# Kernel optimization log

Hardware: AMD Instinct MI355X
Metric: run time of the kernel (lower is better)

The kernel has to match this reference:

```python
import jax, jax.numpy as jnp
import numpy as np
import math

TOP_K = 2
CAPACITY_FACTOR = 1.25


def setup_inputs() -> dict:
    key = jax.random.key(0)
    ks = jax.random.split(key, 5)
    T, H, F, E = 16384, 1024, 4096, 8
    s = lambda d: 1.0 / np.sqrt(d)
    return {
        "tokens": jax.random.normal(ks[0], (T, H), jnp.float32),
        "w_router": jax.random.normal(ks[1], (H, E), jnp.float32) * s(H),
        "w_gate": jax.random.normal(ks[2], (E, H, F), jnp.float32) * s(H),
        "w_up": jax.random.normal(ks[3], (E, H, F), jnp.float32) * s(H),
        "w_down": jax.random.normal(ks[4], (E, F, H), jnp.float32) * s(F),
    }


def _moe_forward(tokens, w_router, w_gate, w_up, w_down):
    T, H = tokens.shape
    E = w_gate.shape[0]
    C = int(math.ceil(CAPACITY_FACTOR * T / E))  # per-expert capacity, static

    # --- Router: softmax over experts, top-k, renormalized weights ---
    logits = tokens @ w_router                       # (T, E)
    probs = jax.nn.softmax(logits, axis=-1)
    topv, topi = jax.lax.top_k(probs, TOP_K)         # (T, K)
    weights = topv / jnp.sum(topv, axis=-1, keepdims=True)

    # --- Dispatch ranks replicating torch loop order: k-slot major, token index minor ---
    onehot = jax.nn.one_hot(topi, E, dtype=jnp.int32)            # (T, K, E)
    counts = onehot.sum(axis=0)                                  # (K, E) tokens per (slot, expert)
    slot_off = jnp.concatenate(
        [jnp.zeros((1, E), jnp.int32), jnp.cumsum(counts, axis=0)[:-1]], axis=0
    )                                                            # (K, E) exclusive offset over k
    rank = jnp.cumsum(onehot, axis=0) - 1 + slot_off[None]       # (T, K, E)
    rank_tk = jnp.take_along_axis(rank, topi[..., None], axis=-1).squeeze(-1)  # (T, K)

    keep = rank_tk < C                                           # tokens beyond capacity are dropped
    slot = jnp.where(keep, rank_tk, C)                           # dropped -> trash slot C

    e_flat = topi.reshape(-1)                                    # (T*K,)
    s_flat = slot.reshape(-1)
    tok_rep = jnp.broadcast_to(tokens[:, None, :], (T, TOP_K, H)).reshape(-1, H)

    # Gather tokens into per-expert capacity buffers (extra trash row at slot C)
    buf = jnp.zeros((E, C + 1, H), tokens.dtype).at[e_flat, s_flat].set(tok_rep)
    x = buf[:, :C]                                               # (E, C, H)

    # --- SwiGLU expert FFN, batched over experts (grouped GEMM) ---
    h = jax.nn.silu(jnp.einsum('ech,ehf->ecf', x, w_gate)) * jnp.einsum('ech,ehf->ecf', x, w_up)
    y = jnp.einsum('ecf,efh->ech', h, w_down)                    # (E, C, H)

    # --- Weighted scatter back to token positions ---
    out_flat = y[e_flat, jnp.minimum(s_flat, C - 1)]             # (T*K, H)
    w_eff = (weights * keep.astype(weights.dtype)).reshape(-1, 1)
    return (out_flat * w_eff).reshape(T, TOP_K, H).sum(axis=1)   # (T, H)


def reference(tokens, w_router, w_gate, w_up, w_down):
    return _moe_forward(tokens, w_router, w_gate, w_up, w_down)
```

## Files before the change

### kernel.cpp

```cpp
#include <hip/hip_runtime.h>
#include <hip/hip_bf16.h>
#include <stdint.h>

#define T_TOK 16384
#define HDIM  1024
#define FDIM  4096
#define NE    8
#define CAP   2560

typedef __attribute__((ext_vector_type(8))) __bf16 bf16x8;
typedef __attribute__((ext_vector_type(4))) float  f32x4;

#define MFMA_BF16 __builtin_amdgcn_mfma_f32_16x16x32_bf16
#define VMCNT3()  asm volatile("s_waitcnt vmcnt(3)" ::: "memory")
#define VMCNT4()  asm volatile("s_waitcnt vmcnt(4)" ::: "memory")
#define LGKM0()   asm volatile("s_waitcnt lgkmcnt(0)" ::: "memory")
#define BAR()     __builtin_amdgcn_s_barrier()
#define SCHED0()  __builtin_amdgcn_sched_barrier(0)

__device__ __forceinline__ unsigned short f2bf(float f) {
  union { float f; unsigned u; } c; c.f = f;
  unsigned u = c.u;
  return (unsigned short)((u + 0x7FFFu + ((u >> 16) & 1u)) >> 16);
}

__device__ __forceinline__ float bf2f(unsigned short u) {
  union { unsigned u; float f; } c; c.u = ((unsigned)u) << 16;
  return c.f;
}

__device__ __forceinline__ void gload_lds16(const void* g, void* lds) {
  __builtin_amdgcn_global_load_lds((const __attribute__((address_space(1))) void*)g,
                                   (__attribute__((address_space(3))) void*)lds,
                                   16, 0, 0);
}

__global__ __launch_bounds__(256)
void transpose_cvt(const float* __restrict__ in, unsigned short* __restrict__ out,
                   int R, int Cc) {
  __shared__ unsigned short tile[64][68];
  int e  = blockIdx.z;
  int rb = blockIdx.y << 6, cb = blockIdx.x << 6;
  const float* inp = in + (size_t)e * R * Cc;
  unsigned short* op = out + (size_t)e * R * Cc;
  int lc  = threadIdx.x & 63;
  int lr0 = threadIdx.x >> 6;
#pragma unroll
  for (int rr = 0; rr < 64; rr += 4) {
    int r = rr + lr0;
    float v = inp[(size_t)(rb + r) * Cc + cb + lc];
    tile[lc][r] = f2bf(v);
  }
  __syncthreads();
  int c0 = threadIdx.x >> 3;
  int h0 = (threadIdx.x & 7) << 3;
#pragma unroll
  for (int cc = 0; cc < 64; cc += 32) {
    int c = cc + c0;
    uint2 v0 = *(const uint2*)&tile[c][h0];
    uint2 v1 = *(const uint2*)&tile[c][h0 + 4];
    uint4 v; v.x = v0.x; v.y = v0.y; v.z = v1.x; v.w = v1.y;
    *(uint4*)(op + (size_t)(cb + c) * R + rb + h0) = v;
  }
}

__global__ __launch_bounds__(256)
void transpose_cvt_gu(const float* __restrict__ in, unsigned short* __restrict__ out, int up) {
  __shared__ unsigned short tile[64][68];
  int e  = blockIdx.z;
  int rb = blockIdx.y << 6, cb = blockIdx.x << 6;
  const float* inp = in + (size_t)e * HDIM * FDIM;
  unsigned short* op = out + (size_t)e * 2 * FDIM * HDIM;
  int lc  = threadIdx.x & 63;
  int lr0 = threadIdx.x >> 6;
#pragma unroll
  for (int rr = 0; rr < 64; rr += 4) {
    int r = rr + lr0;
    float v = inp[(size_t)(rb + r) * FDIM + cb + lc];
    tile[lc][r] = f2bf(v);
  }
  __syncthreads();
  int c0 = threadIdx.x >> 3;
  int h0 = (threadIdx.x & 7) << 3;
#pragma unroll
  for (int cc = 0; cc < 64; cc += 32) {
    int c = cc + c0;
    int C = cb + c;
    int orow = ((C >> 5) << 6) + (C & 31) + (up << 5);
    uint2 v0 = *(const uint2*)&tile[c][h0];
    uint2 v1 = *(const uint2*)&tile[c][h0 + 4];
    uint4 v; v.x = v0.x; v.y = v0.y; v.z = v1.x; v.w = v1.y;
    *(uint4*)(op + (size_t)orow * HDIM + rb + h0) = v;
  }
}

__global__ __launch_bounds__(256)
void router_kernel(const float* __restrict__ tokens, const float* __restrict__ wr,
                   int* __restrict__ topsel, float* __restrict__ wts) {
  int lane = threadIdx.x & 63;
  int t = (blockIdx.x << 2) + (threadIdx.x >> 6);
  const float* tok = tokens + (size_t)t * HDIM;
  float acc[8];
#pragma unroll
  for (int i = 0; i < 8; ++i) acc[i] = 0.f;
#pragma unroll
  for (int j = 0; j < 4; ++j) {
    int h0 = j * 256 + lane * 4;
    float4 tv = *(const float4*)(tok + h0);
    const float* w = wr + (size_t)h0 * 8;
#pragma unroll
    for (int q = 0; q < 4; ++q) {
      float xv = ((const float*)&tv)[q];
      float4 wa = *(const float4*)(w + q * 8);
      float4 wb = *(const float4*)(w + q * 8 + 4);
      acc[0] += xv * wa.x; acc[1] += xv * wa.y; acc[2] += xv * wa.z; acc[3] += xv * wa.w;
      acc[4] += xv * wb.x; acc[5] += xv * wb.y; acc[6] += xv * wb.z; acc[7] += xv * wb.w;
    }
  }
#pragma unroll
  for (int off = 1; off < 64; off <<= 1) {
#pragma unroll
    for (int i = 0; i < 8; ++i) acc[i] += __shfl_xor(acc[i], off, 64);
  }
  if (lane == 0) {
    int e0 = 0; float v0 = acc[0];
#pragma unroll
    for (int i = 1; i < 8; ++i) if (acc[i] > v0) { v0 = acc[i]; e0 = i; }
    int e1 = -1; float v1 = -3.4e38f;
#pragma unroll
    for (int i = 0; i < 8; ++i) if (i != e0 && acc[i] > v1) { v1 = acc[i]; e1 = i; }
    float w0 = 1.f / (1.f + __expf(v1 - v0));
    topsel[t * 2] = e0; topsel[t * 2 + 1] = e1;
    wts[t * 2] = w0;    wts[t * 2 + 1] = 1.f - w0;
  }
}

__global__ __launch_bounds__(256)
void dispatch_kernel(const int* __restrict__ topsel, int* __restrict__ slot,
                     int* __restrict__ src_tok) {
  int e = blockIdx.x;
  int w = threadIdx.x >> 6, lane = threadIdx.x & 63;
  __shared__ int gcnt[2][256];
  __shared__ int tot[2];
#pragma unroll
  for (int k = 0; k < 2; ++k)
    for (int g = w; g < 256; g += 4) {
      int ch = topsel[(g * 64 + lane) * 2 + k];
      unsigned long long m = __ballot(ch == e);
      if (lane == 0) gcnt[k][g] = __popcll(m);
    }
  __syncthreads();
  if (w < 2) {
    int k = w;
    int c0 = gcnt[k][lane * 4], c1 = gcnt[k][lane * 4 + 1];
    int c2 = gcnt[k][lane * 4 + 2], c3 = gcnt[k][lane * 4 + 3];
    int s = c0 + c1 + c2 + c3;
    int inc = s;
#pragma unroll
    for (int off = 1; off < 64; off <<= 1) {
      int v = __shfl_up(inc, off, 64);
      if (lane >= off) inc += v;
    }
    int base = inc - s;
    gcnt[k][lane * 4] = base;
    gcnt[k][lane * 4 + 1] = base + c0;
    gcnt[k][lane * 4 + 2] = base + c0 + c1;
    gcnt[k][lane * 4 + 3] = base + c0 + c1 + c2;
    if (lane == 63) tot[k] = inc;
  }
  __syncthreads();
#pragma unroll
  for (int k = 0; k < 2; ++k) {
    int kbase = (k == 1) ? tot[0] : 0;
    for (int g = w; g < 256; g += 4) {
      int t = g * 64 + lane;
      int ch = topsel[t * 2 + k];
      unsigned long long m = __ballot(ch == e);
      if (ch == e) {
        unsigned long long lmask = lane ? (~0ull >> (64 - lane)) : 0ull;
        int r = kbase + gcnt[k][g] + __popcll(m & lmask);
        if (r < CAP) { slot[t * 2 + k] = r; src_tok[e * CAP + r] = t; }
        else         { slot[t * 2 + k] = -1; }
      }
    }
  }
}

__global__ __launch_bounds__(128)
void gather_x(const float* __restrict__ tokens, const int* __restrict__ src_tok,
              unsigned short* __restrict__ x) {
  int s = blockIdx.x;
  int t = src_tok[s];
  unsigned short* xr = x + (size_t)s * HDIM + threadIdx.x * 8;
  uint4 v = {0u, 0u, 0u, 0u};
  if (t >= 0) {
    const float* tr = tokens + (size_t)t * HDIM + threadIdx.x * 8;
    float4 a = *(const float4*)tr;
    float4 b = *(const float4*)(tr + 4);
    v.x = (unsigned)f2bf(a.x) | ((unsigned)f2bf(a.y) << 16);
    v.y = (unsigned)f2bf(a.z) | ((unsigned)f2bf(a.w) << 16);
    v.z = (unsigned)f2bf(b.x) | ((unsigned)f2bf(b.y) << 16);
    v.w = (unsigned)f2bf(b.z) | ((unsigned)f2bf(b.w) << 16);
  }
  *(uint4*)xr = v;
}

template<int BN>
__device__ __forceinline__ void mainloop8(const unsigned short* __restrict__ Ag,
                                          const unsigned short* __restrict__ Bg,
                                          int lda, int ldb, int nkt,
                                          unsigned short* lds, f32x4 (&acc)[4][BN / 32]) {
  constexpr int NF   = BN / 64;
  constexpr int AELB = 256 * 64 * 2;
  constexpr int BELB = BN * 64 * 2;
  constexpr int BHB  = (BN / 2) * 128;
  int tid = threadIdx.x, lane = tid & 63, wid = tid >> 6;
  int qr = wid >> 1, qc = wid & 1;
  int fr = lane & 15, fg = lane >> 4;

  char* ldsc = (char*)lds;
  int swz0 = ((fg       ^ (fr & 7)) << 4);
  int swz1 = (((4 | fg) ^ (fr & 7)) << 4);
  const char* a_b0 = ldsc + (qr * 32 + fr) * 128 + swz0;
  const char* a_b1 = ldsc + (qr * 32 + fr) * 128 + swz1;
  const char* b_b0 = ldsc + 2 * AELB + (qc * (NF * 16) + fr) * 128 + swz0;
  const char* b_b1 = ldsc + 2 * AELB + (qc * (NF * 16) + fr) * 128 + swz1;

  int srow = tid >> 3;
  int sl8  = ((tid & 7) ^ (srow & 7)) * 8;

  auto stA = [&](int mh, int kt, int pb) {
    char* dst = ldsc + pb + mh * 16384;
    gload_lds16(Ag + (size_t)(mh * 128 + srow) * lda + kt + sl8, dst + tid * 16);
    gload_lds16(Ag + (size_t)(mh * 128 + 64 + srow) * lda + kt + sl8, dst + tid * 16 + 8192);
  };
  auto stB = [&](int nh, int kt, int qb) {
    char* dst = ldsc + 2 * AELB + qb + nh * BHB;
    gload_lds16(Bg + (size_t)(nh * (BN / 2) + srow) * ldb + kt + sl8, dst + tid * 16);
    if constexpr (BN == 256)
      gload_lds16(Bg + (size_t)(nh * (BN / 2) + 64 + srow) * ldb + kt + sl8,
                  dst + tid * 16 + 8192);
  };

  bf16x8 aA[2][2], aB[2][2], bA[NF][2], bB[NF][2];
  auto rdA = [&](bf16x8 (&dst)[2][2], int mh, int pb) {
#pragma unroll
    for (int mf = 0; mf < 2; ++mf) {
      dst[mf][0] = *(const bf16x8*)(a_b0 + pb + mh * 16384 + mf * 2048);
      dst[mf][1] = *(const bf16x8*)(a_b1 + pb + mh * 16384 + mf * 2048);
    }
  };
  auto rdB = [&](bf16x8 (&dst)[NF][2], int nh, int qb) {
#pragma unroll
    for (int nf = 0; nf < NF; ++nf) {
      dst[nf][0] = *(const bf16x8*)(b_b0 + qb + nh * BHB + nf * 2048);
      dst[nf][1] = *(const bf16x8*)(b_b1 + qb + nh * BHB + nf * 2048);
    }
  };
  auto mmq = [&](bf16x8 (&A)[2][2], bf16x8 (&B)[NF][2], int mh, int nh) {
    __builtin_amdgcn_s_setprio(1);
#pragma unroll
    for (int kk = 0; kk < 2; ++kk)
#pragma unroll
      for (int mf = 0; mf < 2; ++mf)
#pragma unroll
        for (int nf = 0; nf < NF; ++nf)
          acc[mh * 2 + mf][nh * NF + nf] =
              MFMA_BF16(A[mf][kk], B[nf][kk], acc[mh * 2 + mf][nh * NF + nf], 0, 0, 0);
    __builtin_amdgcn_s_setprio(0);
  };

  int ktp = (nkt > 1 ? 64 : 0);
  stA(0, 0, 0); stB(0, 0, 0); stA(1, 0, 0); stB(1, 0, 0);
  stA(0, ktp, AELB); stB(1, ktp, BELB);
  if constexpr (BN == 256) VMCNT4(); else VMCNT3();
  BAR();

  for (int t = 0; t < nkt; ++t) {
    int p0 = (t & 1) ? AELB : 0, p1 = AELB - p0;
    int q0 = (t & 1) ? BELB : 0, q1 = BELB - q0;
    int kt1 = ((t + 1 < nkt) ? t + 1 : nkt - 1) * 64;
    int kt2 = ((t + 2 < nkt) ? t + 2 : nkt - 1) * 64;

    rdA(aA, 0, p0); rdB(bA, 0, q0); rdA(aB, 1, p0);
    stB(0, kt1, q1);
    SCHED0();
    LGKM0();
    mmq(aA, bA, 0, 0);
    BAR();

    rdB(bB, 1, q0);
    stA(1, kt1, p1);
    SCHED0();
    mmq(aB, bA, 1, 0);
    LGKM0();
    BAR();

    stA(0, kt2, p0);
    mmq(aB, bB, 1, 1);
    BAR();

    stB(1, kt2, q0);
    mmq(aA, bB, 0, 1);
    if constexpr (BN == 256) VMCNT4(); else VMCNT3();
    BAR();
  }
}

__global__ __launch_bounds__(512, 1)
void gemm1_kernel(const unsigned short* __restrict__ x, const unsigned short* __restrict__ wgu,
                  unsigned short* __restrict__ h) {
  __shared__ unsigned short lds[2 * 256 * 64 + 2 * 256 * 64];
  int flat = blockIdx.x;
  int e = flat & 7, idx = flat >> 3;
  int c = idx >> 4, i = idx & 15;
  int cbx = c / 5, cby = c % 5;
  int bx = cbx * 8 + (i & 7), by = cby * 2 + (i >> 3);
  const unsigned short* Ag = x   + ((size_t)e * CAP + (size_t)by * 256) * HDIM;
  const unsigned short* Bg = wgu + ((size_t)e * 2 * FDIM + (size_t)bx * 256) * HDIM;
  f32x4 acc[4][8];
#pragma unroll
  for (int m = 0; m < 4; ++m)
#pragma unroll
    for (int n = 0; n < 8; ++n) acc[m][n] = (f32x4){0.f, 0.f, 0.f, 0.f};
  mainloop8<256>(Ag, Bg, HDIM, HDIM, HDIM / 64, lds, acc);

  int lane = threadIdx.x & 63, wid = threadIdx.x >> 6;
  int qr = wid >> 1, qc = wid & 1, fr = lane & 15, fg = lane >> 4;
  size_t rbase = (size_t)e * CAP + by * 256;
#pragma unroll
  for (int mi = 0; mi < 4; ++mi) {
    int row0 = (mi >> 1) * 128 + qr * 32 + (mi & 1) * 16 + fg * 4;
#pragma unroll
    for (int nh = 0; nh < 2; ++nh)
#pragma unroll
      for (int nf = 0; nf < 2; ++nf) {
        int fcol = bx * 128 + (nh * 2 + qc) * 32 + nf * 16 + fr;
#pragma unroll
        for (int v = 0; v < 4; ++v) {
          float g = acc[mi][nh * 4 + nf][v];
          float u = acc[mi][nh * 4 + nf + 2][v];
          float s = g / (1.f + __expf(-g));
          h[(rbase + row0 + v) * FDIM + fcol] = f2bf(s * u);
        }
      }
  }
}

__global__ __launch_bounds__(512, 1)
void gemm2_kernel(const unsigned short* __restrict__ h, const unsigned short* __restrict__ wdT,
                  unsigned short* __restrict__ y0, unsigned short* __restrict__ y1) {
  __shared__ unsigned short lds[2 * 256 * 64 + 2 * 256 * 64];
  int flat = blockIdx.x;
  int e = flat & 7, idx = flat >> 3;
  int ks = idx & 1, r2 = idx >> 1;
  int bx = r2 & 3, by = r2 >> 2;
  int k0 = ks * 2048;
  const unsigned short* Ag = h   + ((size_t)e * CAP  + (size_t)by * 256) * FDIM + k0;
  const unsigned short* Bg = wdT + ((size_t)e * HDIM + (size_t)bx * 256) * FDIM + k0;
  f32x4 acc[4][8];
#pragma unroll
  for (int m = 0; m < 4; ++m)
#pragma unroll
    for (int n = 0; n < 8; ++n) acc[m][n] = (f32x4){0.f, 0.f, 0.f, 0.f};
  mainloop8<256>(Ag, Bg, FDIM, FDIM, 2048 / 64, lds, acc);

  unsigned short* yk = ks ? y1 : y0;
  int lane = threadIdx.x & 63, wid = threadIdx.x >> 6;
  int qr = wid >> 1, qc = wid & 1, fr = lane & 15, fg = lane >> 4;
  size_t rbase = (size_t)e * CAP + by * 256;
#pragma unroll
  for (int mi = 0; mi < 4; ++mi) {
    int row0 = (mi >> 1) * 128 + qr * 32 + (mi & 1) * 16 + fg * 4;
#pragma unroll
    for (int nh = 0; nh < 2; ++nh)
#pragma unroll
      for (int nf = 0; nf < 4; ++nf) {
        int col = bx * 256 + nh * 128 + qc * 64 + nf * 16 + fr;
#pragma unroll
        for (int v = 0; v < 4; ++v)
          yk[(rbase + row0 + v) * HDIM + col] = f2bf(acc[mi][nh * 4 + nf][v]);
      }
  }
}

__global__ __launch_bounds__(256)
void combine_kernel(const unsigned short* __restrict__ y0, const unsigned short* __restrict__ y1,
                    const int* __restrict__ topsel, const int* __restrict__ slot,
                    const float* __restrict__ wts, float* __restrict__ out) {
  int t = blockIdx.x;
  int i = threadIdx.x * 4;
  float4 s = {0.f, 0.f, 0.f, 0.f};
#pragma unroll
  for (int k = 0; k < 2; ++k) {
    int sl = slot[t * 2 + k];
    if (sl >= 0) {
      int e = topsel[t * 2 + k];
      float w = wts[t * 2 + k];
      size_t base = ((size_t)e * CAP + sl) * HDIM + i;
      uint2 a = *(const uint2*)(y0 + base);
      uint2 b = *(const uint2*)(y1 + base);
      s.x += w * (bf2f((unsigned short)(a.x & 0xFFFF)) + bf2f((unsigned short)(b.x & 0xFFFF)));
      s.y += w * (bf2f((unsigned short)(a.x >> 16))    + bf2f((unsigned short)(b.x >> 16)));
      s.z += w * (bf2f((unsigned short)(a.y & 0xFFFF)) + bf2f((unsigned short)(b.y & 0xFFFF)));
      s.w += w * (bf2f((unsigned short)(a.y >> 16))    + bf2f((unsigned short)(b.y >> 16)));
    }
  }
  *(float4*)(out + (size_t)t * HDIM + i) = s;
}

extern "C" void kernel_launch(void* const* d_in, const int* in_sizes, int n_in,
                              void* d_out, int out_size, void* d_ws, size_t ws_size,
                              hipStream_t stream) {
  const float* tokens   = (const float*)d_in[0];
  const float* w_router = (const float*)d_in[1];
  const float* w_gate   = (const float*)d_in[2];
  const float* w_up     = (const float*)d_in[3];
  const float* w_down   = (const float*)d_in[4];
  float* out = (float*)d_out;
  char* ws = (char*)d_ws;

  const size_t WGU = (size_t)NE * 2 * FDIM * HDIM * 2;
  const size_t WD  = (size_t)NE * HDIM * FDIM * 2;
  const size_t XB  = (size_t)NE * CAP * HDIM * 2;
  const size_t HB  = (size_t)NE * CAP * FDIM * 2;
  const size_t YB  = (size_t)NE * CAP * HDIM * 2;
  unsigned short* wguT = (unsigned short*)(ws);
  unsigned short* wdT  = (unsigned short*)(ws + WGU);
  unsigned short* xbuf = (unsigned short*)(ws + WGU + WD);
  unsigned short* hbuf = (unsigned short*)(ws + WGU + WD + XB);
  unsigned short* ybuf0 = (unsigned short*)(ws);
  unsigned short* ybuf1 = (unsigned short*)(ws + YB);
  char* tail = ws + WGU + WD + XB + HB;
  int*   topsel  = (int*)tail;
  float* wtsv    = (float*)(tail + (size_t)T_TOK * 2 * 4);
  int*   slotv   = (int*)(tail + (size_t)T_TOK * 2 * 8);
  int*   src_tok = (int*)(tail + (size_t)T_TOK * 2 * 12);

  hipMemsetAsync(src_tok, 0xFF, (size_t)NE * CAP * 4, stream);

  transpose_cvt_gu<<<dim3(FDIM / 64, HDIM / 64, NE), 256, 0, stream>>>(w_gate, wguT, 0);
  transpose_cvt_gu<<<dim3(FDIM / 64, HDIM / 64, NE), 256, 0, stream>>>(w_up,   wguT, 1);
  transpose_cvt<<<dim3(HDIM / 64, FDIM / 64, NE), 256, 0, stream>>>(w_down, wdT, FDIM, HDIM);

  router_kernel<<<T_TOK / 4, 256, 0, stream>>>(tokens, w_router, topsel, wtsv);
  dispatch_kernel<<<NE, 256, 0, stream>>>(topsel, slotv, src_tok);
  gather_x<<<NE * CAP, 128, 0, stream>>>(tokens, src_tok, xbuf);

  gemm1_kernel<<<2560, 512, 0, stream>>>(xbuf, wguT, hbuf);
  gemm2_kernel<<<640, 512, 0, stream>>>(hbuf, wdT, ybuf0, ybuf1);

  combine_kernel<<<T_TOK, 256, 0, stream>>>(ybuf0, ybuf1, topsel, slotv, wtsv, out);
}
```

Before: 746.3 us.

## Load GEMM A operand directly from global into registers, bypass LDS staging

The grouped GEMM mainloop no longer stages the A (activation) tile through LDS. Each wave loads its A fragments directly from global memory into registers, one tile ahead, while B is still double-buffered in LDS. This halves LDS usage and removes the A LDS writes and reads and their waits. In exchange, A global reads are uncoalesced per-lane 16-byte loads that are duplicated across the two column waves, so latency hiding now depends on the new vmcnt thresholds.

Measured after the change: 1.108 ms. +48.5%, slower.

```diff
diff --git a/kernel.cpp b/kernel.cpp
--- a/kernel.cpp
+++ b/kernel.cpp
@@ -12,8 +12,9 @@
 typedef __attribute__((ext_vector_type(4))) float  f32x4;
 
 #define MFMA_BF16 __builtin_amdgcn_mfma_f32_16x16x32_bf16
-#define VMCNT3()  asm volatile("s_waitcnt vmcnt(3)" ::: "memory")
-#define VMCNT4()  asm volatile("s_waitcnt vmcnt(4)" ::: "memory")
+#define VMCNT0()  asm volatile("s_waitcnt vmcnt(0)" ::: "memory")
+#define VMCNT2()  asm volatile("s_waitcnt vmcnt(2)" ::: "memory")
+#define VMCNT10() asm volatile("s_waitcnt vmcnt(10)" ::: "memory")
 #define LGKM0()   asm volatile("s_waitcnt lgkmcnt(0)" ::: "memory")
 #define BAR()     __builtin_amdgcn_s_barrier()
 #define SCHED0()  __builtin_amdgcn_sched_barrier(0)
@@ -205,15 +206,12 @@
   *(uint4*)xr = v;
 }
 
-template<int BN>
-__device__ __forceinline__ void mainloop8(const unsigned short* __restrict__ Ag,
+__device__ __forceinline__ void mainloopA(const unsigned short* __restrict__ Ag,
                                           const unsigned short* __restrict__ Bg,
                                           int lda, int ldb, int nkt,
-                                          unsigned short* lds, f32x4 (&acc)[4][BN / 32]) {
-  constexpr int NF   = BN / 64;
-  constexpr int AELB = 256 * 64 * 2;
-  constexpr int BELB = BN * 64 * 2;
-  constexpr int BHB  = (BN / 2) * 128;
+                                          unsigned short* lds, f32x4 (&acc)[4][8]) {
+  constexpr int BELB = 256 * 64 * 2;
+  constexpr int BHB  = 128 * 128;
   int tid = threadIdx.x, lane = tid & 63, wid = tid >> 6;
   int qr = wid >> 1, qc = wid & 1;
   int fr = lane & 15, fg = lane >> 4;
@@ -221,88 +219,86 @@
   char* ldsc = (char*)lds;
   int swz0 = ((fg       ^ (fr & 7)) << 4);
   int swz1 = (((4 | fg) ^ (fr & 7)) << 4);
-  const char* a_b0 = ldsc + (qr * 32 + fr) * 128 + swz0;
-  const char* a_b1 = ldsc + (qr * 32 + fr) * 128 + swz1;
-  const char* b_b0 = ldsc + 2 * AELB + (qc * (NF * 16) + fr) * 128 + swz0;
-  const char* b_b1 = ldsc + 2 * AELB + (qc * (NF * 16) + fr) * 128 + swz1;
+  const char* b_b0 = ldsc + (qc * 64 + fr) * 128 + swz0;
+  const char* b_b1 = ldsc + (qc * 64 + fr) * 128 + swz1;
 
   int srow = tid >> 3;
   int sl8  = ((tid & 7) ^ (srow & 7)) * 8;
 
-  auto stA = [&](int mh, int kt, int pb) {
-    char* dst = ldsc + pb + mh * 16384;
-    gload_lds16(Ag + (size_t)(mh * 128 + srow) * lda + kt + sl8, dst + tid * 16);
-    gload_lds16(Ag + (size_t)(mh * 128 + 64 + srow) * lda + kt + sl8, dst + tid * 16 + 8192);
+  auto stB = [&](int nh, int kt, int qb) {
+    char* dst = ldsc + qb + nh * BHB;
+    gload_lds16(Bg + (size_t)(nh * 128 + srow) * ldb + kt + sl8, dst + tid * 16);
+    gload_lds16(Bg + (size_t)(nh * 128 + 64 + srow) * ldb + kt + sl8, dst + tid * 16 + 8192);
   };
-  auto stB = [&](int nh, int kt, int qb) {
-    char* dst = ldsc + 2 * AELB + qb + nh * BHB;
-    gload_lds16(Bg + (size_t)(nh * (BN / 2) + srow) * ldb + kt + sl8, dst + tid * 16);
-    if constexpr (BN == 256)
-      gload_lds16(Bg + (size_t)(nh * (BN / 2) + 64 + srow) * ldb + kt + sl8,
-                  dst + tid * 16 + 8192);
+
+  const unsigned short* a00 = Ag + (size_t)(qr * 32 + fr) * lda + fg * 8;
+  const unsigned short* a01 = a00 + 16 * (size_t)lda;
+  const unsigned short* a10 = a00 + 128 * (size_t)lda;
+  const unsigned short* a11 = a00 + 144 * (size_t)lda;
+
+  bf16x8 aA[2][2], aB[2][2], bA[4][2], bB[4][2];
+  auto ldA = [&](bf16x8 (&d)[2][2], const unsigned short* b0, const unsigned short* b1, int kO) {
+    d[0][0] = *(const bf16x8*)(b0 + kO);
+    d[0][1] = *(const bf16x8*)(b0 + kO + 32);
+    d[1][0] = *(const bf16x8*)(b1 + kO);
+    d[1][1] = *(const bf16x8*)(b1 + kO + 32);
   };
-
-  bf16x8 aA[2][2], aB[2][2], bA[NF][2], bB[NF][2];
-  auto rdA = [&](bf16x8 (&dst)[2][2], int mh, int pb) {
-#pragma unroll
-    for (int mf = 0; mf < 2; ++mf) {
-      dst[mf][0] = *(const bf16x8*)(a_b0 + pb + mh * 16384 + mf * 2048);
-      dst[mf][1] = *(const bf16x8*)(a_b1 + pb + mh * 16384 + mf * 2048);
+  auto rdB = [&](bf16x8 (&d)[4][2], int nh, int qb) {
+#pragma unroll
+    for (int nf = 0; nf < 4; ++nf) {
+      d[nf][0] = *(const bf16x8*)(b_b0 + qb + nh * BHB + nf * 2048);
+      d[nf][1] = *(const bf16x8*)(b_b1 + qb + nh * BHB + nf * 2048);
     }
   };
-  auto rdB = [&](bf16x8 (&dst)[NF][2], int nh, int qb) {
-#pragma unroll
-    for (int nf = 0; nf < NF; ++nf) {
-      dst[nf][0] = *(const bf16x8*)(b_b0 + qb + nh * BHB + nf * 2048);
-      dst[nf][1] = *(const bf16x8*)(b_b1 + qb + nh * BHB + nf * 2048);
-    }
-  };
-  auto mmq = [&](bf16x8 (&A)[2][2], bf16x8 (&B)[NF][2], int mh, int nh) {
+  auto mmq = [&](bf16x8 (&A)[2][2], bf16x8 (&B)[4][2], int mh, int nh) {
     __builtin_amdgcn_s_setprio(1);
 #pragma unroll
     for (int kk = 0; kk < 2; ++kk)
 #pragma unroll
       for (int mf = 0; mf < 2; ++mf)
 #pragma unroll
-        for (int nf = 0; nf < NF; ++nf)
-          acc[mh * 2 + mf][nh * NF + nf] =
-              MFMA_BF16(A[mf][kk], B[nf][kk], acc[mh * 2 + mf][nh * NF + nf], 0, 0, 0);
+        for (int nf = 0; nf < 4; ++nf)
+          acc[mh * 2 + mf][nh * 4 + nf] =
+              MFMA_BF16(A[mf][kk], B[nf][kk], acc[mh * 2 + mf][nh * 4 + nf], 0, 0, 0);
     __builtin_amdgcn_s_setprio(0);
   };
 
-  int ktp = (nkt > 1 ? 64 : 0);
-  stA(0, 0, 0); stB(0, 0, 0); stA(1, 0, 0); stB(1, 0, 0);
-  stA(0, ktp, AELB); stB(1, ktp, BELB);
-  if constexpr (BN == 256) VMCNT4(); else VMCNT3();
+  stB(0, 0, 0); stB(1, 0, 0);
+  ldA(aA, a00, a01, 0); ldA(aB, a10, a11, 0);
+  VMCNT0();
   BAR();
 
   for (int t = 0; t < nkt; ++t) {
-    int p0 = (t & 1) ? AELB : 0, p1 = AELB - p0;
     int q0 = (t & 1) ? BELB : 0, q1 = BELB - q0;
     int kt1 = ((t + 1 < nkt) ? t + 1 : nkt - 1) * 64;
-    int kt2 = ((t + 2 < nkt) ? t + 2 : nkt - 1) * 64;
-
-    rdA(aA, 0, p0); rdB(bA, 0, q0); rdA(aB, 1, p0);
+
+    rdB(bA, 0, q0);
     stB(0, kt1, q1);
     SCHED0();
     LGKM0();
+    VMCNT2();
+    SCHED0();
     mmq(aA, bA, 0, 0);
     BAR();
 
     rdB(bB, 1, q0);
-    stA(1, kt1, p1);
+    stB(1, kt1, q1);
     SCHED0();
     mmq(aB, bA, 1, 0);
     LGKM0();
     BAR();
 
-    stA(0, kt2, p0);
     mmq(aB, bB, 1, 1);
+    SCHED0();
+    ldA(aB, a10, a11, kt1);
+    SCHED0();
     BAR();
 
-    stB(1, kt2, q0);
     mmq(aA, bB, 0, 1);
-    if constexpr (BN == 256) VMCNT4(); else VMCNT3();
+    SCHED0();
+    ldA(aA, a00, a01, kt1);
+    SCHED0();
+    VMCNT10();
     BAR();
   }
 }
@@ -310,7 +306,7 @@
 __global__ __launch_bounds__(512, 1)
 void gemm1_kernel(const unsigned short* __restrict__ x, const unsigned short* __restrict__ wgu,
                   unsigned short* __restrict__ h) {
-  __shared__ unsigned short lds[2 * 256 * 64 + 2 * 256 * 64];
+  __shared__ unsigned short lds[2 * 256 * 64];
   int flat = blockIdx.x;
   int e = flat & 7, idx = flat >> 3;
   int c = idx >> 4, i = idx & 15;
@@ -323,7 +319,7 @@
   for (int m = 0; m < 4; ++m)
 #pragma unroll
     for (int n = 0; n < 8; ++n) acc[m][n] = (f32x4){0.f, 0.f, 0.f, 0.f};
-  mainloop8<256>(Ag, Bg, HDIM, HDIM, HDIM / 64, lds, acc);
+  mainloopA(Ag, Bg, HDIM, HDIM, HDIM / 64, lds, acc);
 
   int lane = threadIdx.x & 63, wid = threadIdx.x >> 6;
   int qr = wid >> 1, qc = wid & 1, fr = lane & 15, fg = lane >> 4;
@@ -350,7 +346,7 @@
 __global__ __launch_bounds__(512, 1)
 void gemm2_kernel(const unsigned short* __restrict__ h, const unsigned short* __restrict__ wdT,
                   unsigned short* __restrict__ y0, unsigned short* __restrict__ y1) {
-  __shared__ unsigned short lds[2 * 256 * 64 + 2 * 256 * 64];
+  __shared__ unsigned short lds[2 * 256 * 64];
   int flat = blockIdx.x;
   int e = flat & 7, idx = flat >> 3;
   int ks = idx & 1, r2 = idx >> 1;
@@ -363,7 +359,7 @@
   for (int m = 0; m < 4; ++m)
 #pragma unroll
     for (int n = 0; n < 8; ++n) acc[m][n] = (f32x4){0.f, 0.f, 0.f, 0.f};
-  mainloop8<256>(Ag, Bg, FDIM, FDIM, 2048 / 64, lds, acc);
+  mainloopA(Ag, Bg, FDIM, FDIM, 2048 / 64, lds, acc);
 
   unsigned short* yk = ks ? y1 : y0;
   int lane = threadIdx.x & 63, wid = threadIdx.x >> 6;
```
